# Kernel tuning notes

Measured on AMD Instinct MI355X. Metric: run time of the kernel, lower is better.

The kernel has to match this reference:

```python
import jax, jax.numpy as jnp
import numpy as np

B, P, D = 64, 256, 768
S = P + 1            # class token + patches
GRID = 16.0          # sqrt(no_of_patches)
N_IMGS = 10000


def setup_inputs() -> dict:
    key = jax.random.key(0)
    ks = jax.random.split(key, 10)
    sc = 1.0 / np.sqrt(D)
    return {
        "x": jax.random.normal(ks[0], (B, S, D), jnp.float32),
        "img_ids": jax.random.randint(ks[1], (B,), 0, N_IMGS),
        "mask": jnp.ones((B, S), jnp.int32),
        "avgs": 0.1 * jax.random.normal(ks[2], (N_IMGS, 2, P), jnp.float32),
        "std_devs": jnp.ones((N_IMGS, 2, P), jnp.float32),
        "Wq": sc * jax.random.normal(ks[3], (D, D), jnp.float32),
        "bq": jnp.zeros((D,), jnp.float32),
        "Wk": sc * jax.random.normal(ks[4], (D, D), jnp.float32),
        "bk": jnp.zeros((D,), jnp.float32),
        "Wv": sc * jax.random.normal(ks[5], (D, D), jnp.float32),
        "bv": jnp.zeros((D,), jnp.float32),
        "noise_x": jax.random.normal(ks[6], (B, P), jnp.float32),  # torch.normal(0, sigma)
        "noise_y": jax.random.normal(ks[7], (B, P), jnp.float32),
    }


def reference(x, img_ids, mask, avgs, std_devs, Wq, bq, Wk, bk, Wv, bv, noise_x, noise_y):
    # nn.Linear: y = x @ W^T + b
    q = jnp.einsum("bsd,ed->bse", x, Wq) + bq  # (B,S,D)
    k = jnp.einsum("bsd,ed->bse", x, Wk) + bk
    v = jnp.einsum("bsd,ed->bse", x, Wv) + bv

    a = avgs[img_ids]       # (B,2,P)
    sd = std_devs[img_ids]  # (B,2,P)
    half = (GRID - 1.0) / 2.0
    kx = half * (1.0 + jnp.tanh((noise_x + a[:, 0]) * sd[:, 0]))  # (B,P) in (0, GRID-1)
    ky = half * (1.0 + jnp.tanh((noise_y + a[:, 1]) * sd[:, 1]))
    kx1, kx2 = jnp.ceil(kx), jnp.floor(kx)
    ky1, ky2 = jnp.ceil(ky), jnp.floor(ky)

    # corner order matches original: (x1,y1), (x2,y1), (x1,y2), (x2,y2)
    cx = jnp.stack([kx1, kx2, kx1, kx2], axis=1)  # (B,4,P)
    cy = jnp.stack([ky1, ky1, ky2, ky2], axis=1)
    idxs = jax.lax.stop_gradient(GRID * cy + cx).astype(jnp.int32)  # (B,4,P), < P

    sk = jnp.take_along_axis(k[:, None], idxs[..., None], axis=2)  # (B,4,P,D)
    sv = jnp.take_along_axis(v[:, None], idxs[..., None], axis=2)
    cls = jnp.ones((B, 4, 1, D), sk.dtype)
    skf = jnp.concatenate([cls, sk], axis=2)  # (B,4,S,D)
    svf = jnp.concatenate([cls, sv], axis=2)

    # score per query s against its 4 sampled corner keys; softmax over the 4 corners
    scores = jnp.einsum("bnsd,bsd->bsn", skf, q)   # (B,S,4)
    attn = jax.nn.softmax(scores, axis=-1)          # (B,S,4)
    attn_v = attn.transpose(0, 2, 1)[..., None] * svf  # (B,4,S,D)

    # bilinear weights (1-|cx-kx|)*(1-|cy-ky|); class-token weight fixed to 1
    w = (1.0 - jnp.abs(cx - kx[:, None])) * (1.0 - jnp.abs(cy - ky[:, None]))  # (B,4,P)
    wf = jnp.concatenate([jnp.ones((B, 4, 1), w.dtype), w], axis=2)  # (B,4,S)
    out = jnp.einsum("bns,bnsd->bsd", wf, attn_v)  # (B,S,D)
    return out
```

## Files before the change

kernel.cpp:

```cpp
#include <hip/hip_runtime.h>
#include <math.h>


typedef _Float16 f16x8 __attribute__((ext_vector_type(8)));
typedef _Float16 f16x4 __attribute__((ext_vector_type(4)));
typedef float    f32x4 __attribute__((ext_vector_type(4)));

#define MTOT 16448
#define DD   768
#define NC   2304
#define KT   24
#define XCH (129*24*512)
#define WCH (18*24*512)

__global__ __launch_bounds__(256) void prepass(
    const float* __restrict__ x,
    const float* __restrict__ Wq, const float* __restrict__ Wk, const float* __restrict__ Wv,
    _Float16* __restrict__ xp, _Float16* __restrict__ wp)
{
    const int gidx = blockIdx.x * 256 + threadIdx.x;
    const float* src;
    _Float16* dst;
    if (gidx < XCH) {
        const int c = gidx & 511, kk = (gidx >> 9) % KT, t = gidx / (KT * 512);
        const int row = ((c >> 6) << 4) + (c & 15);
        int gm = t * 128 + row; gm = gm < MTOT ? gm : MTOT - 1;
        src = x + (size_t)gm * DD + kk * 32 + ((c >> 4) & 3) * 8;
        dst = xp + (size_t)gidx * 8;
    } else {
        const int g = gidx - XCH;
        const int c = g & 511, kk = (g >> 9) % KT, t = g / (KT * 512);
        const int wrow = t * 128 + ((c >> 6) << 4) + (c & 15);
        const float* W = wrow < 768 ? Wq : (wrow < 1536 ? Wk : Wv);
        const int srow = wrow - (wrow < 768 ? 0 : (wrow < 1536 ? 768 : 1536));
        src = W + (size_t)srow * DD + kk * 32 + ((c >> 4) & 3) * 8;
        dst = wp + (size_t)g * 8;
    }
    const float4 a = *(const float4*)src;
    const float4 b = *(const float4*)(src + 4);
    f16x8 o;
    o[0] = (_Float16)a.x; o[1] = (_Float16)a.y; o[2] = (_Float16)a.z; o[3] = (_Float16)a.w;
    o[4] = (_Float16)b.x; o[5] = (_Float16)b.y; o[6] = (_Float16)b.z; o[7] = (_Float16)b.w;
    *(f16x8*)dst = o;
}

#define GLD(srcp, ldsp) \
    __builtin_amdgcn_global_load_lds( \
        (const __attribute__((address_space(1))) void*)(srcp), \
        (__attribute__((address_space(3))) void*)(ldsp), 16, 0, 0)

__global__ __launch_bounds__(256) void qkv_gemm(
    const _Float16* __restrict__ xp, const _Float16* __restrict__ wp,
    const float* __restrict__ bq, const float* __restrict__ bk, const float* __restrict__ bv,
    _Float16* __restrict__ qkv)
{
    __shared__ __align__(16) _Float16 Wl[4096];
    __shared__ __align__(16) _Float16 Xl[4096];

    const int bid = blockIdx.x;
    const int xcd = bid & 7, pos = bid >> 3;
    const int q8 = 2322 / 8, r8 = 2322 % 8;
    const int orig = (xcd < r8) ? xcd * (q8 + 1) + pos
                                : r8 * (q8 + 1) + (xcd - r8) * q8 + pos;
    const int xtile = orig / 18, wtile = orig % 18;

    const int tid = threadIdx.x, lane = tid & 63, wid = tid >> 6;
    const int wa = wid >> 1, wb = wid & 1;
    const int r16 = lane & 15, kq = lane >> 4;

    const _Float16* Xsrc = xp + (size_t)xtile * KT * 4096;
    const _Float16* Wsrc = wp + (size_t)wtile * KT * 4096;

    const f32x4 zero = {0.f, 0.f, 0.f, 0.f};
    f32x4 acc[4][4];
    #pragma unroll
    for (int i = 0; i < 4; ++i)
        #pragma unroll
        for (int j = 0; j < 4; ++j) acc[i][j] = zero;

    for (int kk = 0; kk < KT; ++kk) {
        __syncthreads();
        #pragma unroll
        for (int g = 0; g < 2; ++g) {
            const int c0 = g * 256 + wid * 64;
            GLD(Wsrc + ((size_t)kk * 512 + c0 + lane) * 8, &Wl[c0 * 8]);
            GLD(Xsrc + ((size_t)kk * 512 + c0 + lane) * 8, &Xl[c0 * 8]);
        }
        __syncthreads();

        f16x8 a[4], b[4];
        #pragma unroll
        for (int i = 0; i < 4; ++i)
            a[i] = *(const f16x8*)(&Wl[((wa * 4 + i) * 64 + lane) * 8]);
        #pragma unroll
        for (int j = 0; j < 4; ++j)
            b[j] = *(const f16x8*)(&Xl[((wb * 4 + j) * 64 + lane) * 8]);
        #pragma unroll
        for (int i = 0; i < 4; ++i)
            #pragma unroll
            for (int j = 0; j < 4; ++j)
                acc[i][j] = __builtin_amdgcn_mfma_f32_16x16x32_f16(a[i], b[j], acc[i][j], 0, 0, 0);
    }

    const int sec = wtile / 6;
    const float* bias = sec == 0 ? bq : (sec == 1 ? bk : bv);
    #pragma unroll
    for (int i = 0; i < 4; ++i) {
        const int bcol0 = (wtile % 6) * 128 + wa * 64 + i * 16 + kq * 4;
        const int colg0 = wtile * 128 + wa * 64 + i * 16 + kq * 4;
        const float4 bb = *(const float4*)(bias + bcol0);
        #pragma unroll
        for (int j = 0; j < 4; ++j) {
            const int row = xtile * 128 + wb * 64 + j * 16 + r16;
            if (row < MTOT) {
                f16x4 o;
                o[0] = (_Float16)(acc[i][j][0] + bb.x);
                o[1] = (_Float16)(acc[i][j][1] + bb.y);
                o[2] = (_Float16)(acc[i][j][2] + bb.z);
                o[3] = (_Float16)(acc[i][j][3] + bb.w);
                *(f16x4*)(qkv + (size_t)row * NC + colg0) = o;
            }
        }
    }
}

__global__ __launch_bounds__(256) void attn_gather(
    const _Float16* __restrict__ qkv,
    const int*   __restrict__ ids,
    const float* __restrict__ avgs,
    const float* __restrict__ stds,
    const float* __restrict__ nx,
    const float* __restrict__ ny,
    float* __restrict__ out)
{
    const int tid  = threadIdx.x;
    const int lane = tid & 63;
    const int bid = blockIdx.x;
    const int swz = (bid & 7) * 514 + (bid >> 3);
    const int gid = swz * 4 + (tid >> 6);
    const int b = gid / 257, s = gid % 257;
    float* orow = out + (size_t)gid * DD;

    if (s == 0) {
        const float4 one = make_float4(1.f, 1.f, 1.f, 1.f);
        #pragma unroll
        for (int j = 0; j < 3; ++j)
            *(float4*)(orow + 4 * lane + 256 * j) = one;
        return;
    }
    const int p   = s - 1;
    const int img = ids[b];
    const size_t ab = (size_t)img * 512 + p;
    const float a0 = avgs[ab], a1 = avgs[ab + 256];
    const float s0 = stds[ab], s1 = stds[ab + 256];
    const float kx = 7.5f * (1.f + tanhf((nx[b * 256 + p] + a0) * s0));
    const float ky = 7.5f * (1.f + tanhf((ny[b * 256 + p] + a1) * s1));
    const float kx1 = ceilf(kx), kx2 = floorf(kx);
    const float ky1 = ceilf(ky), ky2 = floorf(ky);
    const float cx[4] = {kx1, kx2, kx1, kx2};
    const float cy[4] = {ky1, ky1, ky2, ky2};
    int   idx[4];
    float w[4];
    #pragma unroll
    for (int n = 0; n < 4; ++n) {
        idx[n] = (int)(16.f * cy[n] + cx[n]);
        w[n]   = (1.f - fabsf(cx[n] - kx)) * (1.f - fabsf(cy[n] - ky));
    }

    const _Float16* qrow = qkv + (size_t)gid * NC;
    float qf[12];
    #pragma unroll
    for (int j = 0; j < 3; ++j) {
        const f16x4 v = *(const f16x4*)(qrow + lane * 4 + j * 256);
        qf[4 * j + 0] = (float)v[0]; qf[4 * j + 1] = (float)v[1];
        qf[4 * j + 2] = (float)v[2]; qf[4 * j + 3] = (float)v[3];
    }

    float sc[4];
    #pragma unroll
    for (int n = 0; n < 4; ++n) {
        const _Float16* krow = qkv + (size_t)(b * 257 + idx[n]) * NC + 768;
        float a = 0.f;
        #pragma unroll
        for (int j = 0; j < 3; ++j) {
            const f16x4 kv = *(const f16x4*)(krow + lane * 4 + j * 256);
            a += qf[4 * j + 0] * (float)kv[0] + qf[4 * j + 1] * (float)kv[1]
               + qf[4 * j + 2] * (float)kv[2] + qf[4 * j + 3] * (float)kv[3];
        }
        sc[n] = a;
    }
    #pragma unroll
    for (int n = 0; n < 4; ++n)
        for (int off = 32; off > 0; off >>= 1)
            sc[n] += __shfl_xor(sc[n], off);

    const float mx = fmaxf(fmaxf(sc[0], sc[1]), fmaxf(sc[2], sc[3]));
    const float e0 = expf(sc[0] - mx), e1 = expf(sc[1] - mx),
                e2 = expf(sc[2] - mx), e3 = expf(sc[3] - mx);
    const float inv = 1.f / (e0 + e1 + e2 + e3);
    const float coef[4] = {e0 * inv * w[0], e1 * inv * w[1], e2 * inv * w[2], e3 * inv * w[3]};

    const _Float16* vr0 = qkv + (size_t)(b * 257 + idx[0]) * NC + 1536;
    const _Float16* vr1 = qkv + (size_t)(b * 257 + idx[1]) * NC + 1536;
    const _Float16* vr2 = qkv + (size_t)(b * 257 + idx[2]) * NC + 1536;
    const _Float16* vr3 = qkv + (size_t)(b * 257 + idx[3]) * NC + 1536;
    #pragma unroll
    for (int j = 0; j < 3; ++j) {
        const int d = lane * 4 + j * 256;
        const f16x4 v0 = *(const f16x4*)(vr0 + d);
        const f16x4 v1 = *(const f16x4*)(vr1 + d);
        const f16x4 v2 = *(const f16x4*)(vr2 + d);
        const f16x4 v3 = *(const f16x4*)(vr3 + d);
        float4 o;
        o.x = coef[0] * (float)v0[0] + coef[1] * (float)v1[0] + coef[2] * (float)v2[0] + coef[3] * (float)v3[0];
        o.y = coef[0] * (float)v0[1] + coef[1] * (float)v1[1] + coef[2] * (float)v2[1] + coef[3] * (float)v3[1];
        o.z = coef[0] * (float)v0[2] + coef[1] * (float)v1[2] + coef[2] * (float)v2[2] + coef[3] * (float)v3[2];
        o.w = coef[0] * (float)v0[3] + coef[1] * (float)v1[3] + coef[2] * (float)v2[3] + coef[3] * (float)v3[3];
        *(float4*)(orow + d) = o;
    }
}

extern "C" void kernel_launch(void* const* d_in, const int* in_sizes, int n_in,
                              void* d_out, int out_size, void* d_ws, size_t ws_size,
                              hipStream_t stream) {
    const float* x    = (const float*)d_in[0];
    const int*   ids  = (const int*)  d_in[1];
    const float* avgs = (const float*)d_in[3];
    const float* stds = (const float*)d_in[4];
    const float* Wq   = (const float*)d_in[5];
    const float* bq   = (const float*)d_in[6];
    const float* Wk   = (const float*)d_in[7];
    const float* bk   = (const float*)d_in[8];
    const float* Wv   = (const float*)d_in[9];
    const float* bv   = (const float*)d_in[10];
    const float* nx   = (const float*)d_in[11];
    const float* ny   = (const float*)d_in[12];
    float* out = (float*)d_out;

    char* ws = (char*)d_ws;
    _Float16* qkv = (_Float16*)ws;
    _Float16* xp  = (_Float16*)(ws + 75792384);
    _Float16* wp  = (_Float16*)(ws + 75792384 + 25362432);

    prepass<<<(XCH + WCH) / 256, 256, 0, stream>>>(x, Wq, Wk, Wv, xp, wp);
    qkv_gemm<<<2322, 256, 0, stream>>>(xp, wp, bq, bk, bv, qkv);
    attn_gather<<<4112, 256, 0, stream>>>(qkv, ids, avgs, stds, nx, ny, out);
}
```

Before: 133.4 us.

## Use 8-wave blocks with smaller per-wave tiles in QKV GEMM

Doubles the GEMM block to 512 threads, so each of 8 waves computes a 64x32 sub-tile instead of 4 waves each computing 64x64. The operand roles of the x and W tiles swap, and the epilogue now writes scalar fp16 values per column. The aim is more waves per CU and fewer accumulator registers per wave to hide latency. The trade-off is a less vectorized output store and more A-fragment LDS reads per output.

```diff
diff --git a/kernel.cpp b/kernel.cpp
--- a/kernel.cpp
+++ b/kernel.cpp
@@ -49,76 +49,73 @@
         (const __attribute__((address_space(1))) void*)(srcp), \
         (__attribute__((address_space(3))) void*)(ldsp), 16, 0, 0)
 
-__global__ __launch_bounds__(256) void qkv_gemm(
+__global__ __launch_bounds__(512, 4) void qkv_gemm(
     const _Float16* __restrict__ xp, const _Float16* __restrict__ wp,
     const float* __restrict__ bq, const float* __restrict__ bk, const float* __restrict__ bv,
     _Float16* __restrict__ qkv)
 {
-    __shared__ __align__(16) _Float16 Wl[4096];
-    __shared__ __align__(16) _Float16 Xl[4096];
+    __shared__ __align__(16) _Float16 Ax[4096];
+    __shared__ __align__(16) _Float16 Bx[4096];
 
     const int bid = blockIdx.x;
     const int xcd = bid & 7, pos = bid >> 3;
     const int q8 = 2322 / 8, r8 = 2322 % 8;
     const int orig = (xcd < r8) ? xcd * (q8 + 1) + pos
                                 : r8 * (q8 + 1) + (xcd - r8) * q8 + pos;
-    const int xtile = orig / 18, wtile = orig % 18;
+    const int tileM = orig / 18, tileN = orig % 18;
 
     const int tid = threadIdx.x, lane = tid & 63, wid = tid >> 6;
-    const int wa = wid >> 1, wb = wid & 1;
+    const int wm = wid >> 2, wn = wid & 3;
     const int r16 = lane & 15, kq = lane >> 4;
 
-    const _Float16* Xsrc = xp + (size_t)xtile * KT * 4096;
-    const _Float16* Wsrc = wp + (size_t)wtile * KT * 4096;
+    const _Float16* Asrc = xp + (size_t)tileM * KT * 4096;
+    const _Float16* Bsrc = wp + (size_t)tileN * KT * 4096;
 
     const f32x4 zero = {0.f, 0.f, 0.f, 0.f};
-    f32x4 acc[4][4];
+    f32x4 acc[4][2];
     #pragma unroll
     for (int i = 0; i < 4; ++i)
         #pragma unroll
-        for (int j = 0; j < 4; ++j) acc[i][j] = zero;
+        for (int j = 0; j < 2; ++j) acc[i][j] = zero;
 
     for (int kk = 0; kk < KT; ++kk) {
         __syncthreads();
-        #pragma unroll
-        for (int g = 0; g < 2; ++g) {
-            const int c0 = g * 256 + wid * 64;
-            GLD(Wsrc + ((size_t)kk * 512 + c0 + lane) * 8, &Wl[c0 * 8]);
-            GLD(Xsrc + ((size_t)kk * 512 + c0 + lane) * 8, &Xl[c0 * 8]);
+        {
+            const int c0 = wid * 64;
+            GLD(Asrc + ((size_t)kk * 512 + c0 + lane) * 8, &Ax[c0 * 8]);
+            GLD(Bsrc + ((size_t)kk * 512 + c0 + lane) * 8, &Bx[c0 * 8]);
         }
         __syncthreads();
 
-        f16x8 a[4], b[4];
+        f16x8 a[4], b[2];
         #pragma unroll
         for (int i = 0; i < 4; ++i)
-            a[i] = *(const f16x8*)(&Wl[((wa * 4 + i) * 64 + lane) * 8]);
-        #pragma unroll
-        for (int j = 0; j < 4; ++j)
-            b[j] = *(const f16x8*)(&Xl[((wb * 4 + j) * 64 + lane) * 8]);
+            a[i] = *(const f16x8*)(&Ax[((wm * 4 + i) * 64 + lane) * 8]);
+        #pragma unroll
+        for (int j = 0; j < 2; ++j)
+            b[j] = *(const f16x8*)(&Bx[((wn * 2 + j) * 64 + lane) * 8]);
         #pragma unroll
         for (int i = 0; i < 4; ++i)
             #pragma unroll
-            for (int j = 0; j < 4; ++j)
+            for (int j = 0; j < 2; ++j)
                 acc[i][j] = __builtin_amdgcn_mfma_f32_16x16x32_f16(a[i], b[j], acc[i][j], 0, 0, 0);
     }
 
-    const int sec = wtile / 6;
+    const int sec = tileN / 6;
     const float* bias = sec == 0 ? bq : (sec == 1 ? bk : bv);
+    const int bcol0 = (tileN % 6) * 128 + wn * 32;
     #pragma unroll
     for (int i = 0; i < 4; ++i) {
-        const int bcol0 = (wtile % 6) * 128 + wa * 64 + i * 16 + kq * 4;
-        const int colg0 = wtile * 128 + wa * 64 + i * 16 + kq * 4;
-        const float4 bb = *(const float4*)(bias + bcol0);
-        #pragma unroll
-        for (int j = 0; j < 4; ++j) {
-            const int row = xtile * 128 + wb * 64 + j * 16 + r16;
-            if (row < MTOT) {
-                f16x4 o;
-                o[0] = (_Float16)(acc[i][j][0] + bb.x);
-                o[1] = (_Float16)(acc[i][j][1] + bb.y);
-                o[2] = (_Float16)(acc[i][j][2] + bb.z);
-                o[3] = (_Float16)(acc[i][j][3] + bb.w);
-                *(f16x4*)(qkv + (size_t)row * NC + colg0) = o;
+        const int row0 = tileM * 128 + wm * 64 + i * 16 + kq * 4;
+        #pragma unroll
+        for (int j = 0; j < 2; ++j) {
+            const int col = tileN * 128 + wn * 32 + j * 16 + r16;
+            const float bb = bias[bcol0 + j * 16 + r16];
+            #pragma unroll
+            for (int tt = 0; tt < 4; ++tt) {
+                const int row = row0 + tt;
+                if (row < MTOT)
+                    qkv[(size_t)row * NC + col] = (_Float16)(acc[i][j][tt] + bb);
             }
         }
     }
@@ -243,6 +240,6 @@
     _Float16* wp  = (_Float16*)(ws + 75792384 + 25362432);
 
     prepass<<<(XCH + WCH) / 256, 256, 0, stream>>>(x, Wq, Wk, Wv, xp, wp);
-    qkv_gemm<<<2322, 256, 0, stream>>>(xp, wp, bq, bk, bv, qkv);
+    qkv_gemm<<<2322, 512, 0, stream>>>(xp, wp, bq, bk, bv, qkv);
     attn_gather<<<4112, 256, 0, stream>>>(qkv, ids, avgs, stds, nx, ny, out);
 }
```

New measurement: 120.4 us. 1.11x faster.
